# Performance work log

Hardware: AMD Instinct MI355X
Metric: run time of the kernel (lower is better)

The kernel has to match this reference:

```python
import jax, jax.numpy as jnp
import numpy as np

D_MODEL = 1024
D_STATE = 16
LN_EPS = 1e-5


def setup_inputs() -> dict:
    key = jax.random.key(0)
    ks = jax.random.split(key, 10)
    B, T = 8, 4096
    s = 1.0 / np.sqrt(D_MODEL)
    inp = {
        "x": jax.random.normal(ks[0], (B, T, D_MODEL), jnp.float32),
        "h0": jnp.zeros((B, D_STATE), jnp.float32),
        "mask": jnp.ones((B, T), jnp.float32),
        # params
        "A_diag": -jnp.abs(jax.random.normal(ks[1], (D_STATE,), jnp.float32) * 0.01),
        "W_delta": jax.random.uniform(ks[2], (D_STATE, D_MODEL), jnp.float32, -s, s),
        "W_B": jax.random.uniform(ks[3], (D_STATE, D_MODEL), jnp.float32, -s, s),
        "W_C": jax.random.uniform(ks[4], (D_STATE, D_MODEL), jnp.float32, -s, s),
        "W_out": jax.random.uniform(ks[5], (D_MODEL, D_STATE), jnp.float32, -1/np.sqrt(D_STATE), 1/np.sqrt(D_STATE)),
        "D": jnp.ones((D_MODEL,), jnp.float32),
        "W_gate": jax.random.uniform(ks[6], (D_MODEL, D_MODEL), jnp.float32, -s, s),
        "b_gate": jax.random.uniform(ks[7], (D_MODEL,), jnp.float32, -s, s),
        "ln_w": jnp.ones((D_MODEL,), jnp.float32),
        "ln_b": jnp.zeros((D_MODEL,), jnp.float32),
    }
    return inp


def _layernorm(x, w, b):
    mu = jnp.mean(x, axis=-1, keepdims=True)
    var = jnp.var(x, axis=-1, keepdims=True)
    return (x - mu) * jax.lax.rsqrt(var + LN_EPS) * w + b


def reference(x, h0, mask, A_diag, W_delta, W_B, W_C, W_out, D, W_gate, b_gate, ln_w, ln_b):
    # Per-step projections depend only on x_t -> vectorize over T up front.
    gate = jax.nn.sigmoid(_layernorm(jnp.einsum('btd,ed->bte', x, W_gate) + b_gate, ln_w, ln_b))
    xg = gate * x                                        # [B,T,d_model]
    delta = jax.nn.softplus(jnp.einsum('btd,sd->bts', xg, W_delta))
    Bt = jnp.einsum('btd,sd->bts', xg, W_B)              # [B,T,d_state]
    Ct = jnp.einsum('btd,sd->bts', xg, W_C)
    A_bar = jnp.exp(delta * A_diag)                      # [B,T,d_state]
    m = mask[..., None]                                  # [B,T,1]

    def step(h, inputs):
        a_t, b_t, m_t = inputs                           # [B,ds],[B,ds],[B,1]
        h_cand = jnp.tanh(a_t * h + b_t)
        h_new = h_cand * m_t + h * (1.0 - m_t)
        return h_new, h_new

    # scan over time: move T to leading axis
    h_final, hs = jax.lax.scan(
        step, h0,
        (jnp.swapaxes(A_bar, 0, 1), jnp.swapaxes(Bt, 0, 1), jnp.swapaxes(m, 0, 1)))
    hs = jnp.swapaxes(hs, 0, 1)                          # [B,T,d_state]
    s = Ct * hs
    y = jnp.einsum('bts,ds->btd', s, W_out) + D * x      # [B,T,d_model]
    return (y, h_final)
```

## Files before the change

kernel.cpp:

```cpp
#include <hip/hip_runtime.h>
#include <hip/hip_bf16.h>
#include <cstdint>

#define M_TOK   32768
#define LNEPS   1e-5f
#define TWO_LOG2E 2.8853900817779268f

typedef float  f32x4 __attribute__((ext_vector_type(4)));
typedef short  s16x8 __attribute__((ext_vector_type(8)));

__device__ __forceinline__ unsigned short f2b(float v) {
  return __builtin_bit_cast(unsigned short, __float2bfloat16(v));
}
__device__ __forceinline__ float b2f(unsigned short u) {
  return __bfloat162float(__builtin_bit_cast(__hip_bfloat16, u));
}

__device__ __forceinline__ void async_cp16(const void* g, void* l) {
  using gp = const __attribute__((address_space(1))) char*;
  using lp = __attribute__((address_space(3))) char*;
  __builtin_amdgcn_global_load_lds((gp)(uint64_t)g,
                                   (lp)(uint32_t)(uint64_t)l, 16, 0, 0);
}

__global__ __launch_bounds__(256) void k_convert(
    const float* __restrict__ x, const float* __restrict__ wg,
    const float* __restrict__ wd, const float* __restrict__ wb,
    const float* __restrict__ wc,
    unsigned short* __restrict__ Xb, unsigned short* __restrict__ Wgb,
    unsigned short* __restrict__ Wcat) {
  int i = blockIdx.x * 256 + threadIdx.x;
  const float* src;
  unsigned short* dst;
  if (i < 8388608) {
    src = x + (size_t)i * 4; dst = Xb + (size_t)i * 4;
  } else if (i < 8650752) {
    int j = i - 8388608;
    src = wg + (size_t)j * 4; dst = Wgb + (size_t)j * 4;
  } else {
    int j = i - 8650752;
    int e = j * 4;
    if (e < 16384)       src = wd + e;
    else if (e < 32768)  src = wb + (e - 16384);
    else                 src = wc + (e - 32768);
    dst = Wcat + e;
  }
  float4 v = *(const float4*)src;
  ushort4 o;
  o.x = f2b(v.x); o.y = f2b(v.y); o.z = f2b(v.z); o.w = f2b(v.w);
  *(ushort4*)dst = o;
}

__global__ __launch_bounds__(256, 2) void k_gemm_gate(
    const unsigned short* __restrict__ A,
    const unsigned short* __restrict__ Bm,
    unsigned short* __restrict__ C) {
  __shared__ unsigned short As[128 * 32];
  __shared__ unsigned short Bs[128 * 32];
  const int tid  = threadIdx.x;
  const int wave = tid >> 6, lane = tid & 63;
  const int wr = wave >> 1, wc = wave & 1;
  const int lrow = lane & 15, lq = lane >> 4;
  const int m0 = blockIdx.x * 128;
  const int n0 = blockIdx.y * 128;
  const int crow  = tid >> 2;
  const int ccol  = (tid & 3) * 8;

  f32x4 acc[4][4];
#pragma unroll
  for (int i = 0; i < 4; i++)
#pragma unroll
    for (int j = 0; j < 4; j++) acc[i][j] = (f32x4){0.f, 0.f, 0.f, 0.f};

  for (int k0 = 0; k0 < 1024; k0 += 32) {
    async_cp16(A + (size_t)(m0 + crow) * 1024 + k0 + ccol,
               (void*)(As + (wave * 64) * 8));
    async_cp16(A + (size_t)(m0 + crow + 64) * 1024 + k0 + ccol,
               (void*)(As + (256 + wave * 64) * 8));
    async_cp16(Bm + (size_t)(n0 + crow) * 1024 + k0 + ccol,
               (void*)(Bs + (wave * 64) * 8));
    async_cp16(Bm + (size_t)(n0 + crow + 64) * 1024 + k0 + ccol,
               (void*)(Bs + (256 + wave * 64) * 8));
    __syncthreads();

    s16x8 af[4], bfr[4];
#pragma unroll
    for (int i = 0; i < 4; i++)
      af[i] = *(const s16x8*)(As + (wr * 64 + i * 16 + lrow) * 32 + lq * 8);
#pragma unroll
    for (int j = 0; j < 4; j++)
      bfr[j] = *(const s16x8*)(Bs + (wc * 64 + j * 16 + lrow) * 32 + lq * 8);
#pragma unroll
    for (int i = 0; i < 4; i++)
#pragma unroll
      for (int j = 0; j < 4; j++)
        acc[i][j] = __builtin_amdgcn_mfma_f32_16x16x32_bf16(
            af[i], bfr[j], acc[i][j], 0, 0, 0);
    __syncthreads();
  }

#pragma unroll
  for (int i = 0; i < 4; i++)
#pragma unroll
    for (int j = 0; j < 4; j++)
#pragma unroll
      for (int r = 0; r < 4; r++) {
        int row = m0 + wr * 64 + i * 16 + lq * 4 + r;
        int col = n0 + wc * 64 + j * 16 + lrow;
        C[(size_t)row * 1024 + col] = f2b(acc[i][j][r]);
      }
}

__global__ __launch_bounds__(256) void k_lngate(
    const unsigned short* Gin, const float* __restrict__ x,
    const float* __restrict__ bg, const float* __restrict__ lnw,
    const float* __restrict__ lnb, unsigned short* XG) {
  __shared__ float red[8];
  const int t = threadIdx.x;
  const size_t r = blockIdx.x;
  const int e = t * 4;

  ushort4 g4 = *(const ushort4*)(Gin + r * 1024 + e);
  float4 bg4 = *(const float4*)(bg + e);
  float v0 = b2f(g4.x) + bg4.x;
  float v1 = b2f(g4.y) + bg4.y;
  float v2 = b2f(g4.z) + bg4.z;
  float v3 = b2f(g4.w) + bg4.w;

  float s  = v0 + v1 + v2 + v3;
  float ss = v0 * v0 + v1 * v1 + v2 * v2 + v3 * v3;
#pragma unroll
  for (int off = 32; off >= 1; off >>= 1) {
    s  += __shfl_xor(s, off, 64);
    ss += __shfl_xor(ss, off, 64);
  }
  if ((t & 63) == 0) { red[t >> 6] = s; red[4 + (t >> 6)] = ss; }
  __syncthreads();
  float tot = red[0] + red[1] + red[2] + red[3];
  float tss = red[4] + red[5] + red[6] + red[7];
  float mu  = tot * (1.0f / 1024.0f);
  float var = tss * (1.0f / 1024.0f) - mu * mu;
  float rs  = rsqrtf(var + LNEPS);

  float4 xv = *(const float4*)(x + r * 1024 + e);
  float4 w4 = *(const float4*)(lnw + e);
  float4 b4 = *(const float4*)(lnb + e);
  float u0 = (v0 - mu) * rs * w4.x + b4.x;
  float u1 = (v1 - mu) * rs * w4.y + b4.y;
  float u2 = (v2 - mu) * rs * w4.z + b4.z;
  float u3 = (v3 - mu) * rs * w4.w + b4.w;
  float g0 = 1.0f / (1.0f + __expf(-u0));
  float g1 = 1.0f / (1.0f + __expf(-u1));
  float g2 = 1.0f / (1.0f + __expf(-u2));
  float g3 = 1.0f / (1.0f + __expf(-u3));
  ushort4 o;
  o.x = f2b(g0 * xv.x); o.y = f2b(g1 * xv.y);
  o.z = f2b(g2 * xv.z); o.w = f2b(g3 * xv.w);
  *(ushort4*)(XG + r * 1024 + e) = o;
}

__global__ __launch_bounds__(256) void k_proj(
    const unsigned short* __restrict__ XG, const unsigned short* __restrict__ Wcat,
    const float* __restrict__ A_diag,
    float* __restrict__ UV, float* __restrict__ Ct) {
  __shared__ unsigned short As[64 * 32];
  __shared__ unsigned short Bs[48 * 32];
  const int tid  = threadIdx.x;
  const int wave = tid >> 6, lane = tid & 63;
  const int lrow = lane & 15, lq = lane >> 4;
  const int r0 = blockIdx.x * 64;
  const int crow = tid >> 2, ccol = (tid & 3) * 8;

  f32x4 acc[3];
#pragma unroll
  for (int j = 0; j < 3; j++) acc[j] = (f32x4){0.f, 0.f, 0.f, 0.f};

  for (int k0 = 0; k0 < 1024; k0 += 32) {
    uint4 av = *(const uint4*)(XG + (size_t)(r0 + crow) * 1024 + k0 + ccol);
    uint4 bv;
    if (tid < 192) bv = *(const uint4*)(Wcat + (size_t)crow * 1024 + k0 + ccol);
    __syncthreads();
    *(uint4*)(As + crow * 32 + ccol) = av;
    if (tid < 192) *(uint4*)(Bs + crow * 32 + ccol) = bv;
    __syncthreads();
    s16x8 af = *(const s16x8*)(As + (wave * 16 + lrow) * 32 + lq * 8);
#pragma unroll
    for (int j = 0; j < 3; j++) {
      s16x8 bf8 = *(const s16x8*)(Bs + (j * 16 + lrow) * 32 + lq * 8);
      acc[j] = __builtin_amdgcn_mfma_f32_16x16x32_bf16(af, bf8, acc[j], 0, 0, 0);
    }
  }

  float ad = A_diag[lrow];
#pragma unroll
  for (int r = 0; r < 4; r++) {
    int row = r0 + wave * 16 + lq * 4 + r;
    float z  = acc[0][r];
    float sp = fmaxf(z, 0.0f) + log1pf(__expf(-fabsf(z)));
    float A2 = __expf(sp * ad) * TWO_LOG2E;
    float B2 = acc[1][r] * TWO_LOG2E;
    float2 o;
    o.x = A2 + B2;
    o.y = -2.0f * A2;
    *(float2*)(UV + (size_t)row * 32 + lrow * 2) = o;
    Ct[(size_t)row * 16 + lrow] = acc[2][r];
  }
}

#define TC 128
#define NCH (4096 / TC)

__device__ __forceinline__ void load16(float2 (&P)[16], const float* uvb,
                                       int j, int lane) {
#pragma unroll
  for (int i = 0; i < 16; ++i)
    P[i] = *(const float2*)(uvb + ((j * 16 + i) * 16 + lane) * 2);
}
__device__ __forceinline__ void fast16(float2 (&P)[16], float& r, float& h,
                                       float* hhb, int j, int lane) {
#pragma unroll
  for (int i = 0; i < 16; ++i) {
    float w = fmaf(P[i].y, r, P[i].x);
    float e = __builtin_amdgcn_exp2f(w);
    r = __builtin_amdgcn_rcpf(e + 1.0f);
    h = fmaf(-2.0f, r, 1.0f);
    hhb[(j * 16 + i) * 16 + lane] = h;
  }
}
__device__ __forceinline__ void slow16(float2 (&P)[16], float& h,
                                       const float* mb, float* hhb,
                                       int j, int lane) {
#pragma unroll
  for (int i = 0; i < 16; ++i) {
    float v  = P[i].y, u = P[i].x;
    float A2 = -0.5f * v;
    float B2 = fmaf(0.5f, v, u);
    float w  = fmaf(A2, h, B2);
    float e  = __builtin_amdgcn_exp2f(w);
    float rr = __builtin_amdgcn_rcpf(e + 1.0f);
    float th = fmaf(-2.0f, rr, 1.0f);
    float m  = mb[j * 16 + i];
    h = fmaf(m, th - h, h);
    hhb[(j * 16 + i) * 16 + lane] = h;
  }
}

__global__ __launch_bounds__(512) void k_scan(
    const float* __restrict__ UV, const float* __restrict__ mask,
    const float* __restrict__ h0, float* __restrict__ hs,
    float* __restrict__ hfin) {
  __shared__ float uvL[2][TC * 32];
  __shared__ float hhL[2][TC * 16];
  __shared__ float mskL[2][TC];

  const int tid = threadIdx.x;
  const int b   = blockIdx.x;
  const float* pm = mask + (size_t)b * 4096;
  const size_t uvbase = (size_t)b * 4096 * 32;
  const size_t hsbase = (size_t)b * 4096 * 16;

  float h = 0.f, r = 0.f;
  if (tid < 16) {
    h = h0[b * 16 + tid];
    r = 0.5f - 0.5f * h;
  }

  if (tid >= 64) {
    int pt = tid - 64;
    const uint4* src = (const uint4*)(UV + uvbase);
    for (int i = pt; i < TC * 8; i += 448) ((uint4*)uvL[0])[i] = src[i];
    if (tid < 128) {
      int l = tid - 64;
      mskL[0][l]      = pm[l];
      mskL[0][l + 64] = pm[l + 64];
    }
  }
  __syncthreads();

  for (int c = 0; c < NCH; ++c) {
    const int p = c & 1;
    if (tid < 64) {
      const int lane = tid;
      float mv0 = mskL[p][2 * lane], mv1 = mskL[p][2 * lane + 1];
      bool on = (mv0 == 1.0f) && (mv1 == 1.0f);
      bool allones = (__ballot(on) == 0xFFFFFFFFFFFFFFFFull);
      if (lane < 16) {
        const float* uvb = uvL[p];
        float* hhb = hhL[p];
        float2 Pa[16], Pb[16];
        load16(Pa, uvb, 0, lane);
        if (allones) {
#pragma unroll
          for (int j = 0; j < 8; j += 2) {
            load16(Pb, uvb, j + 1, lane);
            fast16(Pa, r, h, hhb, j, lane);
            if (j + 2 < 8) load16(Pa, uvb, j + 2, lane);
            fast16(Pb, r, h, hhb, j + 1, lane);
          }
        } else {
#pragma unroll
          for (int j = 0; j < 8; j += 2) {
            load16(Pb, uvb, j + 1, lane);
            slow16(Pa, h, mskL[p], hhb, j, lane);
            if (j + 2 < 8) load16(Pa, uvb, j + 2, lane);
            slow16(Pb, h, mskL[p], hhb, j + 1, lane);
          }
          r = 0.5f - 0.5f * h;
        }
      }
    } else {
      int pt = tid - 64;
      if (c + 1 < NCH) {
        const uint4* src =
            (const uint4*)(UV + uvbase + (size_t)(c + 1) * TC * 32);
        uint4* dst = (uint4*)uvL[(c + 1) & 1];
        for (int i = pt; i < TC * 8; i += 448) dst[i] = src[i];
        if (tid < 128) {
          int l = tid - 64;
          mskL[(c + 1) & 1][l]      = pm[(c + 1) * TC + l];
          mskL[(c + 1) & 1][l + 64] = pm[(c + 1) * TC + l + 64];
        }
      }
      if (c > 0) {
        const uint4* s2 = (const uint4*)hhL[(c - 1) & 1];
        uint4* d2 = (uint4*)(hs + hsbase + (size_t)(c - 1) * TC * 16);
        for (int i = pt; i < TC * 4; i += 448) d2[i] = s2[i];
      }
    }
    __syncthreads();
  }

  {
    const uint4* s2 = (const uint4*)hhL[(NCH - 1) & 1];
    uint4* d2 = (uint4*)(hs + hsbase + (size_t)(NCH - 1) * TC * 16);
    if (tid < TC * 4) d2[tid] = s2[tid];
  }
  if (tid < 16) hfin[b * 16 + tid] = h;
}

__global__ __launch_bounds__(256) void k_out(
    const float* __restrict__ Ct, const float* __restrict__ hs,
    const float* __restrict__ Wout, const float* __restrict__ Dd,
    const float* __restrict__ x, float* __restrict__ y) {
  __shared__ float sv[8][16];
  const int t = threadIdx.x;
  const size_t r0 = (size_t)blockIdx.x * 8;
  const int d0 = t * 4;

  float w[4][16];
#pragma unroll
  for (int i = 0; i < 4; i++)
#pragma unroll
    for (int s4 = 0; s4 < 4; s4++)
      *(float4*)&w[i][s4 * 4] = *(const float4*)(Wout + (size_t)(d0 + i) * 16 + s4 * 4);
  float4 D4 = *(const float4*)(Dd + d0);

  if (t < 128) {
    int rr = t >> 4, s = t & 15;
    size_t idx = (r0 + rr) * 16 + s;
    sv[rr][s] = Ct[idx] * hs[idx];
  }
  __syncthreads();

#pragma unroll
  for (int rr = 0; rr < 8; rr++) {
    size_t r = r0 + rr;
    float4 x4 = *(const float4*)(x + r * 1024 + d0);
    float4 o;
    o.x = D4.x * x4.x; o.y = D4.y * x4.y; o.z = D4.z * x4.z; o.w = D4.w * x4.w;
#pragma unroll
    for (int s = 0; s < 16; s++) {
      float svs = sv[rr][s];
      o.x = fmaf(w[0][s], svs, o.x);
      o.y = fmaf(w[1][s], svs, o.y);
      o.z = fmaf(w[2][s], svs, o.z);
      o.w = fmaf(w[3][s], svs, o.w);
    }
    *(float4*)(y + r * 1024 + d0) = o;
  }
}

extern "C" void kernel_launch(void* const* d_in, const int* in_sizes, int n_in,
                              void* d_out, int out_size, void* d_ws, size_t ws_size,
                              hipStream_t stream) {
  const float* x       = (const float*)d_in[0];
  const float* h0      = (const float*)d_in[1];
  const float* mask    = (const float*)d_in[2];
  const float* A_diag  = (const float*)d_in[3];
  const float* W_delta = (const float*)d_in[4];
  const float* W_B     = (const float*)d_in[5];
  const float* W_C     = (const float*)d_in[6];
  const float* W_out   = (const float*)d_in[7];
  const float* Dd      = (const float*)d_in[8];
  const float* W_gate  = (const float*)d_in[9];
  const float* b_gate  = (const float*)d_in[10];
  const float* ln_w    = (const float*)d_in[11];
  const float* ln_b    = (const float*)d_in[12];

  char* ws = (char*)d_ws;
  unsigned short* Xb   = (unsigned short*)(ws);
  unsigned short* Gb   = (unsigned short*)(ws + 67108864);
  unsigned short* Wgb  = (unsigned short*)(ws + 134217728);
  unsigned short* Wcat = (unsigned short*)(ws + 136314880);
  float* UVb = (float*)(ws + 136445952);
  float* Ctb = (float*)(ws + 140640256);
  float* hsb = (float*)(ws + 142737408);

  float* y    = (float*)d_out;
  float* hfin = y + 33554432;

  hipLaunchKernelGGL(k_convert, dim3(33840), dim3(256), 0, stream,
                     x, W_gate, W_delta, W_B, W_C, Xb, Wgb, Wcat);
  hipLaunchKernelGGL(k_gemm_gate, dim3(256, 8), dim3(256), 0, stream, Xb, Wgb, Gb);
  hipLaunchKernelGGL(k_lngate, dim3(32768), dim3(256), 0, stream,
                     Gb, x, b_gate, ln_w, ln_b, Gb);
  hipLaunchKernelGGL(k_proj, dim3(512), dim3(256), 0, stream,
                     Gb, Wcat, A_diag, UVb, Ctb);
  hipLaunchKernelGGL(k_scan, dim3(8), dim3(512), 0, stream,
                     UVb, mask, h0, hsb, hfin);
  hipLaunchKernelGGL(k_out, dim3(4096), dim3(256), 0, stream,
                     Ctb, hsb, W_out, Dd, x, y);
}
```

Measured before the change: 551.4 us.

## Fuse scan and output projection with flag-based chunk streaming; swizzle gate GEMM tiles

```diff
diff --git a/kernel.cpp b/kernel.cpp
--- a/kernel.cpp
+++ b/kernel.cpp
@@ -61,8 +61,10 @@
   const int wave = tid >> 6, lane = tid & 63;
   const int wr = wave >> 1, wc = wave & 1;
   const int lrow = lane & 15, lq = lane >> 4;
-  const int m0 = blockIdx.x * 128;
-  const int n0 = blockIdx.y * 128;
+  const int lin  = blockIdx.y * gridDim.x + blockIdx.x;
+  const int unit = (lin & 7) * 256 + (lin >> 3);
+  const int m0 = (unit >> 3) * 128;
+  const int n0 = (unit & 7) * 128;
   const int crow  = tid >> 2;
   const int ccol  = (tid & 3) * 8;
 
@@ -162,7 +164,7 @@
 __global__ __launch_bounds__(256) void k_proj(
     const unsigned short* __restrict__ XG, const unsigned short* __restrict__ Wcat,
     const float* __restrict__ A_diag,
-    float* __restrict__ UV, float* __restrict__ Ct) {
+    float* __restrict__ UV, float* __restrict__ Ct, int* __restrict__ flags) {
   __shared__ unsigned short As[64 * 32];
   __shared__ unsigned short Bs[48 * 32];
   const int tid  = threadIdx.x;
@@ -170,6 +172,8 @@
   const int lrow = lane & 15, lq = lane >> 4;
   const int r0 = blockIdx.x * 64;
   const int crow = tid >> 2, ccol = (tid & 3) * 8;
+
+  if (blockIdx.x == 0 && tid < 8) flags[tid] = 0;
 
   f32x4 acc[3];
 #pragma unroll
@@ -209,6 +213,7 @@
 
 #define TC 128
 #define NCH (4096 / TC)
+#define NOUT 568
 
 __device__ __forceinline__ void load16(float2 (&P)[16], const float* uvb,
                                        int j, int lane) {
@@ -245,15 +250,67 @@
   }
 }
 
-__global__ __launch_bounds__(512) void k_scan(
+__global__ __launch_bounds__(512, 6) void k_scan_out(
     const float* __restrict__ UV, const float* __restrict__ mask,
     const float* __restrict__ h0, float* __restrict__ hs,
-    float* __restrict__ hfin) {
+    float* __restrict__ hfin,
+    const float* __restrict__ Ct, const float* __restrict__ x,
+    const float* __restrict__ Wout, const float* __restrict__ Dd,
+    float* __restrict__ y, int* __restrict__ flags) {
   __shared__ float uvL[2][TC * 32];
   __shared__ float hhL[2][TC * 16];
   __shared__ float mskL[2][TC];
 
   const int tid = threadIdx.x;
+
+  if (blockIdx.x >= 8) {
+    const int o    = blockIdx.x - 8;
+    const int wv   = tid >> 6;
+    const int lane = tid & 63;
+    const int d0   = wv * 128 + lane * 2;
+
+    float wa[16], wb[16];
+#pragma unroll
+    for (int q = 0; q < 4; q++) {
+      *(float4*)&wa[q * 4] = *(const float4*)(Wout + (size_t)d0 * 16 + q * 4);
+      *(float4*)&wb[q * 4] = *(const float4*)(Wout + (size_t)(d0 + 1) * 16 + q * 4);
+    }
+    float2 D2 = *(const float2*)(Dd + d0);
+
+    for (int c = 0; c < NCH; ++c) {
+      for (int idx = o; idx < 1024; idx += NOUT) {
+        int b = idx >> 7, j = idx & 127;
+        size_t r = (size_t)b * 4096 + (size_t)c * TC + j;
+        int spins = 0;
+        for (;;) {
+          int f = 0;
+          if (lane == 0)
+            f = __hip_atomic_load(&flags[b], __ATOMIC_RELAXED,
+                                  __HIP_MEMORY_SCOPE_AGENT);
+          f = __shfl(f, 0);
+          if (f > c || spins > (1 << 18)) break;
+          ++spins;
+          __builtin_amdgcn_s_sleep(32);
+        }
+        float cv = Ct[r * 16 + (lane & 15)];
+        float hv = __hip_atomic_load(&hs[r * 16 + (lane & 15)],
+                                     __ATOMIC_RELAXED, __HIP_MEMORY_SCOPE_AGENT);
+        float sv = cv * hv;
+        float2 x2 = *(const float2*)(x + r * 1024 + d0);
+        float accx = D2.x * x2.x, accy = D2.y * x2.y;
+#pragma unroll
+        for (int s = 0; s < 16; s++) {
+          float svs = __shfl(sv, s);
+          accx = fmaf(wa[s], svs, accx);
+          accy = fmaf(wb[s], svs, accy);
+        }
+        float2 o2; o2.x = accx; o2.y = accy;
+        *(float2*)(y + r * 1024 + d0) = o2;
+      }
+    }
+    return;
+  }
+
   const int b   = blockIdx.x;
   const float* pm = mask + (size_t)b * 4096;
   const size_t uvbase = (size_t)b * 4096 * 32;
@@ -278,6 +335,11 @@
   __syncthreads();
 
   for (int c = 0; c < NCH; ++c) {
+    if (c >= 2 && tid == 511) {
+      __threadfence();
+      __hip_atomic_store(&flags[b], c - 1, __ATOMIC_RELEASE,
+                         __HIP_MEMORY_SCOPE_AGENT);
+    }
     const int p = c & 1;
     if (tid < 64) {
       const int lane = tid;
@@ -335,49 +397,13 @@
     uint4* d2 = (uint4*)(hs + hsbase + (size_t)(NCH - 1) * TC * 16);
     if (tid < TC * 4) d2[tid] = s2[tid];
   }
+  __syncthreads();
+  if (tid == 511) {
+    __threadfence();
+    __hip_atomic_store(&flags[b], NCH, __ATOMIC_RELEASE,
+                       __HIP_MEMORY_SCOPE_AGENT);
+  }
   if (tid < 16) hfin[b * 16 + tid] = h;
-}
-
-__global__ __launch_bounds__(256) void k_out(
-    const float* __restrict__ Ct, const float* __restrict__ hs,
-    const float* __restrict__ Wout, const float* __restrict__ Dd,
-    const float* __restrict__ x, float* __restrict__ y) {
-  __shared__ float sv[8][16];
-  const int t = threadIdx.x;
-  const size_t r0 = (size_t)blockIdx.x * 8;
-  const int d0 = t * 4;
-
-  float w[4][16];
-#pragma unroll
-  for (int i = 0; i < 4; i++)
-#pragma unroll
-    for (int s4 = 0; s4 < 4; s4++)
-      *(float4*)&w[i][s4 * 4] = *(const float4*)(Wout + (size_t)(d0 + i) * 16 + s4 * 4);
-  float4 D4 = *(const float4*)(Dd + d0);
-
-  if (t < 128) {
-    int rr = t >> 4, s = t & 15;
-    size_t idx = (r0 + rr) * 16 + s;
-    sv[rr][s] = Ct[idx] * hs[idx];
-  }
-  __syncthreads();
-
-#pragma unroll
-  for (int rr = 0; rr < 8; rr++) {
-    size_t r = r0 + rr;
-    float4 x4 = *(const float4*)(x + r * 1024 + d0);
-    float4 o;
-    o.x = D4.x * x4.x; o.y = D4.y * x4.y; o.z = D4.z * x4.z; o.w = D4.w * x4.w;
-#pragma unroll
-    for (int s = 0; s < 16; s++) {
-      float svs = sv[rr][s];
-      o.x = fmaf(w[0][s], svs, o.x);
-      o.y = fmaf(w[1][s], svs, o.y);
-      o.z = fmaf(w[2][s], svs, o.z);
-      o.w = fmaf(w[3][s], svs, o.w);
-    }
-    *(float4*)(y + r * 1024 + d0) = o;
-  }
 }
 
 extern "C" void kernel_launch(void* const* d_in, const int* in_sizes, int n_in,
@@ -402,6 +428,7 @@
   unsigned short* Gb   = (unsigned short*)(ws + 67108864);
   unsigned short* Wgb  = (unsigned short*)(ws + 134217728);
   unsigned short* Wcat = (unsigned short*)(ws + 136314880);
+  int* flags = (int*)(ws + 136413184);
   float* UVb = (float*)(ws + 136445952);
   float* Ctb = (float*)(ws + 140640256);
   float* hsb = (float*)(ws + 142737408);
@@ -415,9 +442,7 @@
   hipLaunchKernelGGL(k_lngate, dim3(32768), dim3(256), 0, stream,
                      Gb, x, b_gate, ln_w, ln_b, Gb);
   hipLaunchKernelGGL(k_proj, dim3(512), dim3(256), 0, stream,
-                     Gb, Wcat, A_diag, UVb, Ctb);
-  hipLaunchKernelGGL(k_scan, dim3(8), dim3(512), 0, stream,
-                     UVb, mask, h0, hsb, hfin);
-  hipLaunchKernelGGL(k_out, dim3(4096), dim3(256), 0, stream,
-                     Ctb, hsb, W_out, Dd, x, y);
-}
+                     Gb, Wcat, A_diag, UVb, Ctb, flags);
+  hipLaunchKernelGGL(k_scan_out, dim3(8 + NOUT), dim3(512), 0, stream,
+                     UVb, mask, h0, hsb, hfin, Ctb, x, W_out, Dd, y, flags);
+}
```

After: 525.4 us. -4.7%, faster.
